# Kernel tuning notes

Hardware: AMD Instinct MI355X
Metric: run time of the kernel (lower is better)

## Reference

```python
import jax, jax.numpy as jnp
import numpy as np

DIM, HEADS, FEAT = 512, 8, 128
HEAD_DIM = DIM // HEADS
B, N = 1, 2048
EPS = 1e-8


def setup_inputs() -> dict:
    key = jax.random.key(0)
    k1, k2, k3, k4 = jax.random.split(key, 4)
    x = jax.random.normal(k1, (B, N, DIM), dtype=jnp.float32)
    proj_matrix = jax.random.normal(k2, (HEADS, HEAD_DIM, FEAT), dtype=jnp.float32) / np.sqrt(HEAD_DIM)
    W_qkv = jax.random.normal(k3, (DIM, 3 * DIM), dtype=jnp.float32) * np.sqrt(2.0 / DIM)
    W_out = jax.random.normal(k4, (DIM, DIM), dtype=jnp.float32) * np.sqrt(2.0 / DIM)
    b_out = jnp.zeros((DIM,), dtype=jnp.float32)
    return {"x": x, "proj_matrix": proj_matrix, "W_qkv": W_qkv, "W_out": W_out, "b_out": b_out}


def _feature_map(t):
    return jax.nn.elu(t) + 1.0


def reference(x, proj_matrix, W_qkv, W_out, b_out):
    b, n, d = x.shape
    h, hd = HEADS, HEAD_DIM
    qkv = x @ W_qkv                      # (b,n,3d)
    q, k, v = jnp.split(qkv, 3, axis=-1)
    # (b,n,d) -> (b,h,n,hd)
    def to_heads(t):
        return t.reshape(b, n, h, hd).transpose(0, 2, 1, 3)
    q, k, v = to_heads(q), to_heads(k), to_heads(v)
    q_proj = _feature_map(jnp.einsum('bhnd,hdf->bhnf', q, proj_matrix))
    k_proj = _feature_map(jnp.einsum('bhnd,hdf->bhnf', k, proj_matrix))
    # causal linear attention via prefix sums (matches torch cumsum branch)
    k_cum = jnp.cumsum(k_proj, axis=2)                                   # (b,h,n,f)
    kv_cum = jnp.cumsum(k_proj[..., None] * v[..., None, :], axis=2)     # (b,h,n,f,hd)
    attn = jnp.einsum('bhnf,bhnfd->bhnd', q_proj, kv_cum)
    denom = jnp.einsum('bhnf,bhnf->bhn', q_proj, k_cum)[..., None]
    attn = attn / (denom + EPS)
    attn = attn.transpose(0, 2, 1, 3).reshape(b, n, d)
    return attn @ W_out + b_out
```

## Files before the change

### kernel.cpp

```cpp
#include <hip/hip_runtime.h>
#include <math.h>

#define NTOK 2048
#define DMODEL 512
#define NH 8
#define HD 64
#define NF 128
#define QKV_LD 1536
#define CHUNK 64
#define NCHUNK 32
#define EPS_C 1e-8f

typedef __bf16 bf16x8 __attribute__((ext_vector_type(8)));
typedef float f32x4 __attribute__((ext_vector_type(4)));

__device__ inline unsigned short f2bf(float f) {
  union { float f; unsigned u; } v; v.f = f;
  unsigned r = v.u + 0x7FFF + ((v.u >> 16) & 1);
  return (unsigned short)(r >> 16);
}


__global__ __launch_bounds__(256) void pack_all(
    const float* __restrict__ x, const float* __restrict__ W_qkv,
    const float* __restrict__ W_out, const float* __restrict__ proj,
    unsigned short* __restrict__ xpk, unsigned short* __restrict__ wqkvpk,
    unsigned short* __restrict__ woutpk, unsigned short* __restrict__ projpk,
    unsigned short* __restrict__ vT_pk)
{
  const int tid = blockIdx.x * 256 + threadIdx.x;
  const int job = blockIdx.y;
  unsigned short o[8];
  if (job == 0) {
    if (tid >= 131072) return;
    const int lane = tid & 63, blk = tid >> 6;
    const int bk = blk & 15, bm = blk >> 4;
    const int m = bm * 16 + (lane & 15), k = bk * 32 + (lane >> 4) * 8;
    const float4 v0 = *(const float4*)&x[(size_t)m * 512 + k];
    const float4 v1 = *(const float4*)&x[(size_t)m * 512 + k + 4];
    o[0] = f2bf(v0.x); o[1] = f2bf(v0.y); o[2] = f2bf(v0.z); o[3] = f2bf(v0.w);
    o[4] = f2bf(v1.x); o[5] = f2bf(v1.y); o[6] = f2bf(v1.z); o[7] = f2bf(v1.w);
    *(ushort4*)&xpk[(size_t)tid * 8]     = *(ushort4*)&o[0];
    *(ushort4*)&xpk[(size_t)tid * 8 + 4] = *(ushort4*)&o[4];
  } else if (job == 1) {
    if (tid >= 98304) return;
    const int lane = tid & 63, blk = tid >> 6;
    const int bk = blk & 15, bn = blk >> 4;
    const int n = bn * 16 + (lane & 15), k = bk * 32 + (lane >> 4) * 8;
#pragma unroll
    for (int e = 0; e < 8; ++e) o[e] = f2bf(W_qkv[(size_t)(k + e) * QKV_LD + n]);
    *(ushort4*)&wqkvpk[(size_t)tid * 8]     = *(ushort4*)&o[0];
    *(ushort4*)&wqkvpk[(size_t)tid * 8 + 4] = *(ushort4*)&o[4];
  } else if (job == 2) {
    if (tid >= 32768) return;
    const int lane = tid & 63, blk = tid >> 6;
    const int bk = blk & 15, bn = blk >> 4;
    const int n = bn * 16 + (lane & 15), k = bk * 32 + (lane >> 4) * 8;
#pragma unroll
    for (int e = 0; e < 8; ++e) o[e] = f2bf(W_out[(size_t)(k + e) * DMODEL + n]);
    *(ushort4*)&woutpk[(size_t)tid * 8]     = *(ushort4*)&o[0];
    *(ushort4*)&woutpk[(size_t)tid * 8 + 4] = *(ushort4*)&o[4];
  } else if (job == 3) {
    if (tid >= 8192) return;
    const int lane = tid & 63, blk = (tid >> 6) & 15, h = tid >> 10;
    const int bk = blk & 1, bn = blk >> 1;
    const int n = bn * 16 + (lane & 15), k = bk * 32 + (lane >> 4) * 8;
#pragma unroll
    for (int e = 0; e < 8; ++e) o[e] = f2bf(proj[(size_t)h * HD * NF + (size_t)(k + e) * NF + n]);
    *(ushort4*)&projpk[(size_t)tid * 8]     = *(ushort4*)&o[0];
    *(ushort4*)&projpk[(size_t)tid * 8 + 4] = *(ushort4*)&o[4];
  } else {
    if (tid >= 32768) return;
    const int hc = tid >> 7, kt = (tid >> 6) & 1, lane = tid & 63;
    const unsigned short val = ((lane & 15) == 0) ? (unsigned short)0x3F80 : (unsigned short)0;
    const size_t u = (size_t)hc * 640 + (4 * 2 + kt) * 64 + lane;
#pragma unroll
    for (int e = 0; e < 8; ++e) o[e] = val;
    *(ushort4*)&vT_pk[u * 8]     = *(ushort4*)&o[0];
    *(ushort4*)&vT_pk[u * 8 + 4] = *(ushort4*)&o[4];
  }
}

__global__ __launch_bounds__(256) void qkv_proj(
    const unsigned short* __restrict__ Apk, const unsigned short* __restrict__ Bpk,
    const unsigned short* __restrict__ projpk,
    unsigned short* __restrict__ q_pk, unsigned short* __restrict__ k_pk,
    unsigned short* __restrict__ kT_pk, unsigned short* __restrict__ vT_pk)
{
  __shared__ unsigned short QK[4096];
  const int lane = threadIdx.x & 63, w = threadIdx.x >> 6;
  const int wr = w >> 1, wc = w & 1;
  const int c = blockIdx.y;
  const int m0 = c * 64 + wr * 32;
  const int n0 = blockIdx.x * 64 + wc * 32;
  const unsigned short* a0 = Apk + ((size_t)(m0 >> 4) * 16 * 64 + lane) * 8;
  const unsigned short* a1 = a0 + (size_t)16 * 512;
  const unsigned short* b0 = Bpk + ((size_t)(n0 >> 4) * 16 * 64 + lane) * 8;
  const unsigned short* b1 = b0 + (size_t)16 * 512;
  f32x4 acc00 = {0.f, 0.f, 0.f, 0.f}, acc01 = acc00, acc10 = acc00, acc11 = acc00;
#pragma unroll 4
  for (int s = 0; s < 16; ++s) {
    const bf16x8 af0 = *(const bf16x8*)(a0 + (size_t)s * 512);
    const bf16x8 af1 = *(const bf16x8*)(a1 + (size_t)s * 512);
    const bf16x8 bv0 = *(const bf16x8*)(b0 + (size_t)s * 512);
    const bf16x8 bv1 = *(const bf16x8*)(b1 + (size_t)s * 512);
    acc00 = __builtin_amdgcn_mfma_f32_16x16x32_bf16(af0, bv0, acc00, 0, 0, 0);
    acc01 = __builtin_amdgcn_mfma_f32_16x16x32_bf16(af0, bv1, acc01, 0, 0, 0);
    acc10 = __builtin_amdgcn_mfma_f32_16x16x32_bf16(af1, bv0, acc10, 0, 0, 0);
    acc11 = __builtin_amdgcn_mfma_f32_16x16x32_bf16(af1, bv1, acc11, 0, 0, 0);
  }
  const int r16 = lane & 15, kg = lane >> 4;
  if (blockIdx.x < 16) {
    const int src = blockIdx.x >> 3, h = blockIdx.x & 7;
#pragma unroll
    for (int mb = 0; mb < 2; ++mb) {
#pragma unroll
      for (int nb = 0; nb < 2; ++nb) {
        const f32x4 a = mb == 0 ? (nb == 0 ? acc00 : acc01) : (nb == 0 ? acc10 : acc11);
        const size_t u = ((size_t)(wr * 2 + mb) * 2 + wc) * 64 +
                         (nb * 2 + (r16 >> 3)) * 16 + kg * 4;
        const int elem = r16 & 7;
#pragma unroll
        for (int r = 0; r < 4; ++r)
          QK[(u + r) * 8 + elem] = f2bf(a[r]);
      }
    }
    __syncthreads();
    const unsigned short* bbase = projpk + (size_t)h * 8192 + (size_t)lane * 8;
    f32x4 p[2][4] = {};
#pragma unroll
    for (int s = 0; s < 2; ++s) {
#pragma unroll
      for (int mb = 0; mb < 2; ++mb) {
        const bf16x8 af = *(const bf16x8*)&QK[((((size_t)(wr * 2 + mb)) * 2 + s) * 64 + lane) * 8];
#pragma unroll
        for (int nb = 0; nb < 4; ++nb) {
          const bf16x8 bv = *(const bf16x8*)(bbase + (size_t)((wc * 4 + nb) * 2 + s) * 512);
          p[mb][nb] = __builtin_amdgcn_mfma_f32_16x16x32_bf16(af, bv, p[mb][nb], 0, 0, 0);
        }
      }
    }
    unsigned short* dst = (src ? k_pk : q_pk) + (size_t)h * 262144;
#pragma unroll
    for (int mb = 0; mb < 2; ++mb) {
#pragma unroll
      for (int nb = 0; nb < 4; ++nb) {
        unsigned short vb[4];
#pragma unroll
        for (int r = 0; r < 4; ++r) {
          const float v = p[mb][nb][r];
          vb[r] = f2bf(v > 0.f ? v + 1.f : expf(v));
        }
        const size_t base = ((size_t)(c * 4 + wr * 2 + mb) * 4 + wc * 2 + (nb >> 1)) * 64 +
                            ((nb & 1) * 2 + (r16 >> 3)) * 16;
        const int elem = r16 & 7;
#pragma unroll
        for (int r = 0; r < 4; ++r)
          dst[(base + kg * 4 + r) * 8 + elem] = vb[r];
        if (src == 1) {
          const size_t u = (size_t)(h * 32 + c) * 1024 +
              ((size_t)(wc * 4 + nb) * 2 + wr) * 64 + r16 + (mb * 2 + (kg >> 1)) * 16;
          *(ushort4*)&kT_pk[u * 8 + (kg & 1) * 4] = *(ushort4*)&vb[0];
        }
      }
    }
  } else {
    const int h = blockIdx.x - 16;
#pragma unroll
    for (int mb = 0; mb < 2; ++mb) {
#pragma unroll
      for (int nb = 0; nb < 2; ++nb) {
        const f32x4 a = mb == 0 ? (nb == 0 ? acc00 : acc01) : (nb == 0 ? acc10 : acc11);
        const int vc = wc * 32 + nb * 16 + r16;
        const size_t u = (size_t)(h * 32 + c) * 640 +
            ((size_t)(vc >> 4) * 2 + wr) * 64 + (vc & 15) + (mb * 2 + (kg >> 1)) * 16;
        ushort4 rr;
        rr.x = f2bf(a[0]); rr.y = f2bf(a[1]); rr.z = f2bf(a[2]); rr.w = f2bf(a[3]);
        *(ushort4*)&vT_pk[u * 8 + (kg & 1) * 4] = rr;
      }
    }
  }
}

__global__ __launch_bounds__(256) void sums_scan(
    const unsigned short* __restrict__ kT_pk, const unsigned short* __restrict__ vT_pk,
    unsigned short* __restrict__ kvpre_pk)
{
  const int lane = threadIdx.x & 63, w = threadIdx.x >> 6;
  const int vt = blockIdx.x, h = blockIdx.y;
  const int r16 = lane & 15, kg = lane >> 4;
  f32x4 acc[2] = {};
  for (int c = 0; c < NCHUNK; ++c) {
    unsigned short* dst = kvpre_pk + (size_t)(h * 32 + c) * 1280 * 8;
#pragma unroll
    for (int mb = 0; mb < 2; ++mb) {
      unsigned short vb[4];
#pragma unroll
      for (int r = 0; r < 4; ++r) vb[r] = f2bf(acc[mb][r]);
      const size_t u = (size_t)(vt * 4 + w) * 64 + r16 + (mb * 2 + (kg >> 1)) * 16;
      *(ushort4*)&dst[u * 8 + (kg & 1) * 4] = *(ushort4*)&vb[0];
    }
    const unsigned short* kb = kT_pk + (size_t)(h * 32 + c) * 1024 * 8;
    const unsigned short* vb_ = vT_pk + (size_t)(h * 32 + c) * 640 * 8;
#pragma unroll
    for (int s = 0; s < 2; ++s) {
      const bf16x8 bf = *(const bf16x8*)(vb_ + (((size_t)vt * 2 + s) * 64 + lane) * 8);
#pragma unroll
      for (int mb = 0; mb < 2; ++mb) {
        const bf16x8 af = *(const bf16x8*)(kb + ((((size_t)(w * 2 + mb)) * 2 + s) * 64 + lane) * 8);
        acc[mb] = __builtin_amdgcn_mfma_f32_16x16x32_bf16(af, bf, acc[mb], 0, 0, 0);
      }
    }
  }
}

__global__ __launch_bounds__(256) void gemm_out(
    const unsigned short* __restrict__ Apk, const unsigned short* __restrict__ Bpk,
    const float* __restrict__ bias, float* __restrict__ Cf, int K, int ldc)
{
  const int lane = threadIdx.x & 63, w = threadIdx.x >> 6;
  const int wr = w >> 1, wc = w & 1;
  const int m0 = blockIdx.y * 64 + wr * 32;
  const int n0 = blockIdx.x * 64 + wc * 32;
  const int ks = K >> 5;
  const unsigned short* a0 = Apk + ((size_t)(m0 >> 4) * ks * 64 + lane) * 8;
  const unsigned short* a1 = a0 + (size_t)ks * 512;
  const unsigned short* b0 = Bpk + ((size_t)(n0 >> 4) * ks * 64 + lane) * 8;
  const unsigned short* b1 = b0 + (size_t)ks * 512;
  f32x4 acc00 = {0.f, 0.f, 0.f, 0.f}, acc01 = acc00, acc10 = acc00, acc11 = acc00;
#pragma unroll 4
  for (int s = 0; s < ks; ++s) {
    const bf16x8 af0 = *(const bf16x8*)(a0 + (size_t)s * 512);
    const bf16x8 af1 = *(const bf16x8*)(a1 + (size_t)s * 512);
    const bf16x8 bv0 = *(const bf16x8*)(b0 + (size_t)s * 512);
    const bf16x8 bv1 = *(const bf16x8*)(b1 + (size_t)s * 512);
    acc00 = __builtin_amdgcn_mfma_f32_16x16x32_bf16(af0, bv0, acc00, 0, 0, 0);
    acc01 = __builtin_amdgcn_mfma_f32_16x16x32_bf16(af0, bv1, acc01, 0, 0, 0);
    acc10 = __builtin_amdgcn_mfma_f32_16x16x32_bf16(af1, bv0, acc10, 0, 0, 0);
    acc11 = __builtin_amdgcn_mfma_f32_16x16x32_bf16(af1, bv1, acc11, 0, 0, 0);
  }
  const int r16 = lane & 15, kg = lane >> 4;
#pragma unroll
  for (int mb = 0; mb < 2; ++mb) {
#pragma unroll
    for (int nb = 0; nb < 2; ++nb) {
      const f32x4 a = mb == 0 ? (nb == 0 ? acc00 : acc01) : (nb == 0 ? acc10 : acc11);
      const int col = n0 + nb * 16 + r16;
      const float bv = bias[col];
#pragma unroll
      for (int r = 0; r < 4; ++r)
        Cf[(size_t)(m0 + mb * 16 + kg * 4 + r) * ldc + col] = a[r] + bv;
    }
  }
}

__global__ __launch_bounds__(256) void chunk_attn(
    const unsigned short* __restrict__ q_pk, const unsigned short* __restrict__ k_pk,
    const unsigned short* __restrict__ kvpre_pk, const unsigned short* __restrict__ vT_pk,
    unsigned short* __restrict__ attn_pk)
{
  __shared__ unsigned short P[4096];
  __shared__ float den[64];
  const int lane = threadIdx.x & 63, w = threadIdx.x >> 6;
  const int wr = w >> 1, wc = w & 1;
  const int c = blockIdx.x, h = blockIdx.y;
  const int r16 = lane & 15, kg = lane >> 4;
  const unsigned short* qb = q_pk + (size_t)h * 262144;
  const unsigned short* kb = k_pk + (size_t)h * 262144;
  bf16x8 qa[2][4];
#pragma unroll
  for (int amb = 0; amb < 2; ++amb)
#pragma unroll
    for (int ks = 0; ks < 4; ++ks)
      qa[amb][ks] = *(const bf16x8*)(qb +
          (((size_t)(c * 4 + wr * 2 + amb) * 4 + ks) * 64 + lane) * 8);
  {
    f32x4 accS[2][2] = {};
#pragma unroll
    for (int ks = 0; ks < 4; ++ks) {
#pragma unroll
      for (int bnb = 0; bnb < 2; ++bnb) {
        const bf16x8 bf = *(const bf16x8*)(kb +
            (((size_t)(c * 4 + wc * 2 + bnb) * 4 + ks) * 64 + lane) * 8);
#pragma unroll
        for (int amb = 0; amb < 2; ++amb)
          accS[amb][bnb] = __builtin_amdgcn_mfma_f32_16x16x32_bf16(qa[amb][ks], bf, accS[amb][bnb], 0, 0, 0);
      }
    }
#pragma unroll
    for (int amb = 0; amb < 2; ++amb)
#pragma unroll
      for (int bnb = 0; bnb < 2; ++bnb) {
        const int ck = wc * 32 + bnb * 16 + r16;
        const size_t u = ((size_t)(wr * 2 + amb) * 2 + wc) * 64 + (bnb * 2 + (r16 >> 3)) * 16;
        const int elem = r16 & 7;
#pragma unroll
        for (int r = 0; r < 4; ++r) {
          const int rq = wr * 32 + amb * 16 + kg * 4 + r;
          P[(u + kg * 4 + r) * 8 + elem] = (ck <= rq) ? f2bf(accS[amb][bnb][r]) : (unsigned short)0;
        }
      }
  }
  __syncthreads();
  const int nnt = wc ? 2 : 3;
  const int ntb = wc ? 3 : 0;
  const unsigned short* kvp = kvpre_pk + (size_t)(h * 32 + c) * 1280 * 8;
  const unsigned short* vtb = vT_pk + (size_t)(h * 32 + c) * 640 * 8;
  f32x4 acc[2][3] = {};
#pragma unroll
  for (int ks = 0; ks < 4; ++ks) {
    bf16x8 bfr[3];
    for (int j = 0; j < 3; ++j)
      if (j < nnt)
        bfr[j] = *(const bf16x8*)(kvp + (((size_t)(ntb + j) * 4 + ks) * 64 + lane) * 8);
#pragma unroll
    for (int amb = 0; amb < 2; ++amb)
      for (int j = 0; j < 3; ++j)
        if (j < nnt)
          acc[amb][j] = __builtin_amdgcn_mfma_f32_16x16x32_bf16(qa[amb][ks], bfr[j], acc[amb][j], 0, 0, 0);
  }
#pragma unroll
  for (int ks = 0; ks < 2; ++ks) {
    bf16x8 bfr[3];
    for (int j = 0; j < 3; ++j)
      if (j < nnt)
        bfr[j] = *(const bf16x8*)(vtb + (((size_t)(ntb + j) * 2 + ks) * 64 + lane) * 8);
#pragma unroll
    for (int amb = 0; amb < 2; ++amb) {
      const bf16x8 pf = *(const bf16x8*)&P[((((size_t)(wr * 2 + amb)) * 2 + ks) * 64 + lane) * 8];
      for (int j = 0; j < 3; ++j)
        if (j < nnt)
          acc[amb][j] = __builtin_amdgcn_mfma_f32_16x16x32_bf16(pf, bfr[j], acc[amb][j], 0, 0, 0);
    }
  }
  if (wc == 1 && r16 == 0) {
#pragma unroll
    for (int amb = 0; amb < 2; ++amb)
#pragma unroll
      for (int r = 0; r < 4; ++r)
        den[wr * 32 + amb * 16 + kg * 4 + r] = acc[amb][1][r] + EPS_C;
  }
  __syncthreads();
#pragma unroll
  for (int amb = 0; amb < 2; ++amb) {
    for (int j = 0; j < 3; ++j) {
      const int nt = ntb + j;
      if (nt >= 4 || j >= nnt) continue;
      const int acol = h * 64 + nt * 16 + r16;
      const size_t base = ((size_t)(c * 4 + wr * 2 + amb) * 16 + (acol >> 5)) * 64 +
                          ((nt * 2 + (r16 >> 3)) & 3) * 16;
      const int elem = acol & 7;
#pragma unroll
      for (int r = 0; r < 4; ++r) {
        const float dinv = 1.0f / den[wr * 32 + amb * 16 + kg * 4 + r];
        attn_pk[(base + kg * 4 + r) * 8 + elem] = f2bf(acc[amb][j][r] * dinv);
      }
    }
  }
}

extern "C" void kernel_launch(void* const* d_in, const int* in_sizes, int n_in,
                              void* d_out, int out_size, void* d_ws, size_t ws_size,
                              hipStream_t stream) {
  const float* x     = (const float*)d_in[0];
  const float* proj  = (const float*)d_in[1];
  const float* W_qkv = (const float*)d_in[2];
  const float* W_out = (const float*)d_in[3];
  const float* b_out = (const float*)d_in[4];
  float* out = (float*)d_out;

  unsigned short* xpk      = (unsigned short*)d_ws;
  unsigned short* wqkvpk   = xpk + 1048576;
  unsigned short* woutpk   = wqkvpk + 786432;
  unsigned short* projpk   = woutpk + 262144;
  unsigned short* q_pk     = projpk + 65536;
  unsigned short* k_pk     = q_pk + 2097152;
  unsigned short* kT_pk    = k_pk + 2097152;
  unsigned short* vT_pk    = kT_pk + 2097152;
  unsigned short* kvpre_pk = vT_pk + 1310720;
  unsigned short* attn_pk  = kvpre_pk + 2621440;

  pack_all<<<dim3(512, 5), 256, 0, stream>>>(x, W_qkv, W_out, proj,
                                             xpk, wqkvpk, woutpk, projpk, vT_pk);
  qkv_proj<<<dim3(QKV_LD / 64, NTOK / 64), 256, 0, stream>>>(
      xpk, wqkvpk, projpk, q_pk, k_pk, kT_pk, vT_pk);
  sums_scan<<<dim3(5, NH), 256, 0, stream>>>(kT_pk, vT_pk, kvpre_pk);
  chunk_attn<<<dim3(NCHUNK, NH), 256, 0, stream>>>(
      q_pk, k_pk, kvpre_pk, vT_pk, attn_pk);
  gemm_out<<<dim3(DMODEL / 64, NTOK / 64), 256, 0, stream>>>(
      attn_pk, woutpk, b_out, out, DMODEL, DMODEL);
}
```

Measured before the change: 52.56 us.

## Flatten pack grid, split chunk attention by row half, raise GEMM unroll

```diff
diff --git a/kernel.cpp b/kernel.cpp
--- a/kernel.cpp
+++ b/kernel.cpp
@@ -21,18 +21,17 @@
 }
 
 
-__global__ __launch_bounds__(256) void pack_all(
+__global__ __launch_bounds__(256) void pack_flat(
     const float* __restrict__ x, const float* __restrict__ W_qkv,
     const float* __restrict__ W_out, const float* __restrict__ proj,
     unsigned short* __restrict__ xpk, unsigned short* __restrict__ wqkvpk,
     unsigned short* __restrict__ woutpk, unsigned short* __restrict__ projpk,
     unsigned short* __restrict__ vT_pk)
 {
-  const int tid = blockIdx.x * 256 + threadIdx.x;
-  const int job = blockIdx.y;
+  const int v = blockIdx.x;
   unsigned short o[8];
-  if (job == 0) {
-    if (tid >= 131072) return;
+  if (v < 512) {
+    const int tid = v * 256 + threadIdx.x;
     const int lane = tid & 63, blk = tid >> 6;
     const int bk = blk & 15, bm = blk >> 4;
     const int m = bm * 16 + (lane & 15), k = bk * 32 + (lane >> 4) * 8;
@@ -42,8 +41,8 @@
     o[4] = f2bf(v1.x); o[5] = f2bf(v1.y); o[6] = f2bf(v1.z); o[7] = f2bf(v1.w);
     *(ushort4*)&xpk[(size_t)tid * 8]     = *(ushort4*)&o[0];
     *(ushort4*)&xpk[(size_t)tid * 8 + 4] = *(ushort4*)&o[4];
-  } else if (job == 1) {
-    if (tid >= 98304) return;
+  } else if (v < 896) {
+    const int tid = (v - 512) * 256 + threadIdx.x;
     const int lane = tid & 63, blk = tid >> 6;
     const int bk = blk & 15, bn = blk >> 4;
     const int n = bn * 16 + (lane & 15), k = bk * 32 + (lane >> 4) * 8;
@@ -51,8 +50,8 @@
     for (int e = 0; e < 8; ++e) o[e] = f2bf(W_qkv[(size_t)(k + e) * QKV_LD + n]);
     *(ushort4*)&wqkvpk[(size_t)tid * 8]     = *(ushort4*)&o[0];
     *(ushort4*)&wqkvpk[(size_t)tid * 8 + 4] = *(ushort4*)&o[4];
-  } else if (job == 2) {
-    if (tid >= 32768) return;
+  } else if (v < 1024) {
+    const int tid = (v - 896) * 256 + threadIdx.x;
     const int lane = tid & 63, blk = tid >> 6;
     const int bk = blk & 15, bn = blk >> 4;
     const int n = bn * 16 + (lane & 15), k = bk * 32 + (lane >> 4) * 8;
@@ -60,8 +59,8 @@
     for (int e = 0; e < 8; ++e) o[e] = f2bf(W_out[(size_t)(k + e) * DMODEL + n]);
     *(ushort4*)&woutpk[(size_t)tid * 8]     = *(ushort4*)&o[0];
     *(ushort4*)&woutpk[(size_t)tid * 8 + 4] = *(ushort4*)&o[4];
-  } else if (job == 3) {
-    if (tid >= 8192) return;
+  } else if (v < 1056) {
+    const int tid = (v - 1024) * 256 + threadIdx.x;
     const int lane = tid & 63, blk = (tid >> 6) & 15, h = tid >> 10;
     const int bk = blk & 1, bn = blk >> 1;
     const int n = bn * 16 + (lane & 15), k = bk * 32 + (lane >> 4) * 8;
@@ -70,7 +69,7 @@
     *(ushort4*)&projpk[(size_t)tid * 8]     = *(ushort4*)&o[0];
     *(ushort4*)&projpk[(size_t)tid * 8 + 4] = *(ushort4*)&o[4];
   } else {
-    if (tid >= 32768) return;
+    const int tid = (v - 1056) * 256 + threadIdx.x;
     const int hc = tid >> 7, kt = (tid >> 6) & 1, lane = tid & 63;
     const unsigned short val = ((lane & 15) == 0) ? (unsigned short)0x3F80 : (unsigned short)0;
     const size_t u = (size_t)hc * 640 + (4 * 2 + kt) * 64 + lane;
@@ -98,7 +97,7 @@
   const unsigned short* b0 = Bpk + ((size_t)(n0 >> 4) * 16 * 64 + lane) * 8;
   const unsigned short* b1 = b0 + (size_t)16 * 512;
   f32x4 acc00 = {0.f, 0.f, 0.f, 0.f}, acc01 = acc00, acc10 = acc00, acc11 = acc00;
-#pragma unroll 4
+#pragma unroll 8
   for (int s = 0; s < 16; ++s) {
     const bf16x8 af0 = *(const bf16x8*)(a0 + (size_t)s * 512);
     const bf16x8 af1 = *(const bf16x8*)(a1 + (size_t)s * 512);
@@ -148,8 +147,8 @@
         unsigned short vb[4];
 #pragma unroll
         for (int r = 0; r < 4; ++r) {
-          const float v = p[mb][nb][r];
-          vb[r] = f2bf(v > 0.f ? v + 1.f : expf(v));
+          const float vv = p[mb][nb][r];
+          vb[r] = f2bf(vv > 0.f ? vv + 1.f : expf(vv));
         }
         const size_t base = ((size_t)(c * 4 + wr * 2 + mb) * 4 + wc * 2 + (nb >> 1)) * 64 +
                             ((nb & 1) * 2 + (r16 >> 3)) * 16;
@@ -209,6 +208,110 @@
       for (int mb = 0; mb < 2; ++mb) {
         const bf16x8 af = *(const bf16x8*)(kb + ((((size_t)(w * 2 + mb)) * 2 + s) * 64 + lane) * 8);
         acc[mb] = __builtin_amdgcn_mfma_f32_16x16x32_bf16(af, bf, acc[mb], 0, 0, 0);
+      }
+    }
+  }
+}
+
+__global__ __launch_bounds__(128) void chunk_attn2(
+    const unsigned short* __restrict__ q_pk, const unsigned short* __restrict__ k_pk,
+    const unsigned short* __restrict__ kvpre_pk, const unsigned short* __restrict__ vT_pk,
+    unsigned short* __restrict__ attn_pk)
+{
+  __shared__ unsigned short P[2048];
+  __shared__ float den[32];
+  const int lane = threadIdx.x & 63, wc = threadIdx.x >> 6;
+  const int c = blockIdx.x, h = blockIdx.y, rh = blockIdx.z;
+  const int r16 = lane & 15, kg = lane >> 4;
+  const unsigned short* qb = q_pk + (size_t)h * 262144;
+  const unsigned short* kb = k_pk + (size_t)h * 262144;
+  bf16x8 qa[2][4];
+#pragma unroll
+  for (int amb = 0; amb < 2; ++amb)
+#pragma unroll
+    for (int ks = 0; ks < 4; ++ks)
+      qa[amb][ks] = *(const bf16x8*)(qb +
+          (((size_t)(c * 4 + rh * 2 + amb) * 4 + ks) * 64 + lane) * 8);
+  {
+    f32x4 accS[2][2] = {};
+#pragma unroll
+    for (int ks = 0; ks < 4; ++ks) {
+#pragma unroll
+      for (int bnb = 0; bnb < 2; ++bnb) {
+        const bf16x8 bf = *(const bf16x8*)(kb +
+            (((size_t)(c * 4 + wc * 2 + bnb) * 4 + ks) * 64 + lane) * 8);
+#pragma unroll
+        for (int amb = 0; amb < 2; ++amb)
+          accS[amb][bnb] = __builtin_amdgcn_mfma_f32_16x16x32_bf16(qa[amb][ks], bf, accS[amb][bnb], 0, 0, 0);
+      }
+    }
+#pragma unroll
+    for (int amb = 0; amb < 2; ++amb)
+#pragma unroll
+      for (int bnb = 0; bnb < 2; ++bnb) {
+        const int ck = wc * 32 + bnb * 16 + r16;
+        const size_t u = ((size_t)amb * 2 + wc) * 64 + (bnb * 2 + (r16 >> 3)) * 16;
+        const int elem = r16 & 7;
+#pragma unroll
+        for (int r = 0; r < 4; ++r) {
+          const int rq = rh * 32 + amb * 16 + kg * 4 + r;
+          P[(u + kg * 4 + r) * 8 + elem] = (ck <= rq) ? f2bf(accS[amb][bnb][r]) : (unsigned short)0;
+        }
+      }
+  }
+  __syncthreads();
+  const int nnt = wc ? 2 : 3;
+  const int ntb = wc ? 3 : 0;
+  const unsigned short* kvp = kvpre_pk + (size_t)(h * 32 + c) * 1280 * 8;
+  const unsigned short* vtb = vT_pk + (size_t)(h * 32 + c) * 640 * 8;
+  f32x4 acc[2][3] = {};
+#pragma unroll
+  for (int ks = 0; ks < 4; ++ks) {
+    bf16x8 bfr[3];
+    for (int jj = 0; jj < 3; ++jj)
+      if (jj < nnt)
+        bfr[jj] = *(const bf16x8*)(kvp + (((size_t)(ntb + jj) * 4 + ks) * 64 + lane) * 8);
+#pragma unroll
+    for (int amb = 0; amb < 2; ++amb)
+      for (int jj = 0; jj < 3; ++jj)
+        if (jj < nnt)
+          acc[amb][jj] = __builtin_amdgcn_mfma_f32_16x16x32_bf16(qa[amb][ks], bfr[jj], acc[amb][jj], 0, 0, 0);
+  }
+#pragma unroll
+  for (int ks = 0; ks < 2; ++ks) {
+    bf16x8 bfr[3];
+    for (int jj = 0; jj < 3; ++jj)
+      if (jj < nnt)
+        bfr[jj] = *(const bf16x8*)(vtb + (((size_t)(ntb + jj) * 2 + ks) * 64 + lane) * 8);
+#pragma unroll
+    for (int amb = 0; amb < 2; ++amb) {
+      const bf16x8 pf = *(const bf16x8*)&P[(((size_t)amb * 2 + ks) * 64 + lane) * 8];
+      for (int jj = 0; jj < 3; ++jj)
+        if (jj < nnt)
+          acc[amb][jj] = __builtin_amdgcn_mfma_f32_16x16x32_bf16(pf, bfr[jj], acc[amb][jj], 0, 0, 0);
+    }
+  }
+  if (wc == 1 && r16 == 0) {
+#pragma unroll
+    for (int amb = 0; amb < 2; ++amb)
+#pragma unroll
+      for (int r = 0; r < 4; ++r)
+        den[amb * 16 + kg * 4 + r] = acc[amb][1][r] + EPS_C;
+  }
+  __syncthreads();
+#pragma unroll
+  for (int amb = 0; amb < 2; ++amb) {
+    for (int jj = 0; jj < 3; ++jj) {
+      const int nt = ntb + jj;
+      if (nt >= 4 || jj >= nnt) continue;
+      const int acol = h * 64 + nt * 16 + r16;
+      const size_t base = ((size_t)(c * 4 + rh * 2 + amb) * 16 + (acol >> 5)) * 64 +
+                          ((nt * 2 + (r16 >> 3)) & 3) * 16;
+      const int elem = acol & 7;
+#pragma unroll
+      for (int r = 0; r < 4; ++r) {
+        const float dinv = 1.0f / den[amb * 16 + kg * 4 + r];
+        attn_pk[(base + kg * 4 + r) * 8 + elem] = f2bf(acc[amb][jj][r] * dinv);
       }
     }
   }
@@ -228,7 +331,7 @@
   const unsigned short* b0 = Bpk + ((size_t)(n0 >> 4) * ks * 64 + lane) * 8;
   const unsigned short* b1 = b0 + (size_t)ks * 512;
   f32x4 acc00 = {0.f, 0.f, 0.f, 0.f}, acc01 = acc00, acc10 = acc00, acc11 = acc00;
-#pragma unroll 4
+#pragma unroll 8
   for (int s = 0; s < ks; ++s) {
     const bf16x8 af0 = *(const bf16x8*)(a0 + (size_t)s * 512);
     const bf16x8 af1 = *(const bf16x8*)(a1 + (size_t)s * 512);
@@ -250,111 +353,6 @@
 #pragma unroll
       for (int r = 0; r < 4; ++r)
         Cf[(size_t)(m0 + mb * 16 + kg * 4 + r) * ldc + col] = a[r] + bv;
-    }
-  }
-}
-
-__global__ __launch_bounds__(256) void chunk_attn(
-    const unsigned short* __restrict__ q_pk, const unsigned short* __restrict__ k_pk,
-    const unsigned short* __restrict__ kvpre_pk, const unsigned short* __restrict__ vT_pk,
-    unsigned short* __restrict__ attn_pk)
-{
-  __shared__ unsigned short P[4096];
-  __shared__ float den[64];
-  const int lane = threadIdx.x & 63, w = threadIdx.x >> 6;
-  const int wr = w >> 1, wc = w & 1;
-  const int c = blockIdx.x, h = blockIdx.y;
-  const int r16 = lane & 15, kg = lane >> 4;
-  const unsigned short* qb = q_pk + (size_t)h * 262144;
-  const unsigned short* kb = k_pk + (size_t)h * 262144;
-  bf16x8 qa[2][4];
-#pragma unroll
-  for (int amb = 0; amb < 2; ++amb)
-#pragma unroll
-    for (int ks = 0; ks < 4; ++ks)
-      qa[amb][ks] = *(const bf16x8*)(qb +
-          (((size_t)(c * 4 + wr * 2 + amb) * 4 + ks) * 64 + lane) * 8);
-  {
-    f32x4 accS[2][2] = {};
-#pragma unroll
-    for (int ks = 0; ks < 4; ++ks) {
-#pragma unroll
-      for (int bnb = 0; bnb < 2; ++bnb) {
-        const bf16x8 bf = *(const bf16x8*)(kb +
-            (((size_t)(c * 4 + wc * 2 + bnb) * 4 + ks) * 64 + lane) * 8);
-#pragma unroll
-        for (int amb = 0; amb < 2; ++amb)
-          accS[amb][bnb] = __builtin_amdgcn_mfma_f32_16x16x32_bf16(qa[amb][ks], bf, accS[amb][bnb], 0, 0, 0);
-      }
-    }
-#pragma unroll
-    for (int amb = 0; amb < 2; ++amb)
-#pragma unroll
-      for (int bnb = 0; bnb < 2; ++bnb) {
-        const int ck = wc * 32 + bnb * 16 + r16;
-        const size_t u = ((size_t)(wr * 2 + amb) * 2 + wc) * 64 + (bnb * 2 + (r16 >> 3)) * 16;
-        const int elem = r16 & 7;
-#pragma unroll
-        for (int r = 0; r < 4; ++r) {
-          const int rq = wr * 32 + amb * 16 + kg * 4 + r;
-          P[(u + kg * 4 + r) * 8 + elem] = (ck <= rq) ? f2bf(accS[amb][bnb][r]) : (unsigned short)0;
-        }
-      }
-  }
-  __syncthreads();
-  const int nnt = wc ? 2 : 3;
-  const int ntb = wc ? 3 : 0;
-  const unsigned short* kvp = kvpre_pk + (size_t)(h * 32 + c) * 1280 * 8;
-  const unsigned short* vtb = vT_pk + (size_t)(h * 32 + c) * 640 * 8;
-  f32x4 acc[2][3] = {};
-#pragma unroll
-  for (int ks = 0; ks < 4; ++ks) {
-    bf16x8 bfr[3];
-    for (int j = 0; j < 3; ++j)
-      if (j < nnt)
-        bfr[j] = *(const bf16x8*)(kvp + (((size_t)(ntb + j) * 4 + ks) * 64 + lane) * 8);
-#pragma unroll
-    for (int amb = 0; amb < 2; ++amb)
-      for (int j = 0; j < 3; ++j)
-        if (j < nnt)
-          acc[amb][j] = __builtin_amdgcn_mfma_f32_16x16x32_bf16(qa[amb][ks], bfr[j], acc[amb][j], 0, 0, 0);
-  }
-#pragma unroll
-  for (int ks = 0; ks < 2; ++ks) {
-    bf16x8 bfr[3];
-    for (int j = 0; j < 3; ++j)
-      if (j < nnt)
-        bfr[j] = *(const bf16x8*)(vtb + (((size_t)(ntb + j) * 2 + ks) * 64 + lane) * 8);
-#pragma unroll
-    for (int amb = 0; amb < 2; ++amb) {
-      const bf16x8 pf = *(const bf16x8*)&P[((((size_t)(wr * 2 + amb)) * 2 + ks) * 64 + lane) * 8];
-      for (int j = 0; j < 3; ++j)
-        if (j < nnt)
-          acc[amb][j] = __builtin_amdgcn_mfma_f32_16x16x32_bf16(pf, bfr[j], acc[amb][j], 0, 0, 0);
-    }
-  }
-  if (wc == 1 && r16 == 0) {
-#pragma unroll
-    for (int amb = 0; amb < 2; ++amb)
-#pragma unroll
-      for (int r = 0; r < 4; ++r)
-        den[wr * 32 + amb * 16 + kg * 4 + r] = acc[amb][1][r] + EPS_C;
-  }
-  __syncthreads();
-#pragma unroll
-  for (int amb = 0; amb < 2; ++amb) {
-    for (int j = 0; j < 3; ++j) {
-      const int nt = ntb + j;
-      if (nt >= 4 || j >= nnt) continue;
-      const int acol = h * 64 + nt * 16 + r16;
-      const size_t base = ((size_t)(c * 4 + wr * 2 + amb) * 16 + (acol >> 5)) * 64 +
-                          ((nt * 2 + (r16 >> 3)) & 3) * 16;
-      const int elem = acol & 7;
-#pragma unroll
-      for (int r = 0; r < 4; ++r) {
-        const float dinv = 1.0f / den[wr * 32 + amb * 16 + kg * 4 + r];
-        attn_pk[(base + kg * 4 + r) * 8 + elem] = f2bf(acc[amb][j][r] * dinv);
-      }
     }
   }
 }
@@ -380,12 +378,12 @@
   unsigned short* kvpre_pk = vT_pk + 1310720;
   unsigned short* attn_pk  = kvpre_pk + 2621440;
 
-  pack_all<<<dim3(512, 5), 256, 0, stream>>>(x, W_qkv, W_out, proj,
-                                             xpk, wqkvpk, woutpk, projpk, vT_pk);
+  pack_flat<<<dim3(1184), 256, 0, stream>>>(x, W_qkv, W_out, proj,
+                                            xpk, wqkvpk, woutpk, projpk, vT_pk);
   qkv_proj<<<dim3(QKV_LD / 64, NTOK / 64), 256, 0, stream>>>(
       xpk, wqkvpk, projpk, q_pk, k_pk, kT_pk, vT_pk);
   sums_scan<<<dim3(5, NH), 256, 0, stream>>>(kT_pk, vT_pk, kvpre_pk);
-  chunk_attn<<<dim3(NCHUNK, NH), 256, 0, stream>>>(
+  chunk_attn2<<<dim3(NCHUNK, NH, 2), 128, 0, stream>>>(
       q_pk, k_pk, kvpre_pk, vT_pk, attn_pk);
   gemm_out<<<dim3(DMODEL / 64, NTOK / 64), 256, 0, stream>>>(
       attn_pk, woutpk, b_out, out, DMODEL, DMODEL);
```

Measured after the change: 53.19 us. No clear change (+1.2%).
